# Optimization experiments

Hardware: AMD Instinct MI355X
Metric: run time of the kernel (lower is better)

The kernel has to match this reference:

```python
import jax, jax.numpy as jnp
from jax import lax
import numpy as np

ALPHA = 0.5   # combined weight on dice loss
BETA = 0.5    # combined weight on boundary loss; NOTE: BoundaryLoss also multiplies by beta internally, so boundary term gets beta**2 overall (faithful to the torch code)
SMOOTH = 1e-06
BIG = 1e6     # 'infinity' for 1D distance scans (>> H+W)


def _dist1d_last(mask):
    """1D distance (in pixels) to nearest True along the last axis of [B,H,W]."""
    m = jnp.moveaxis(mask, 2, 0)  # [W,B,H]
    init = jnp.full(m.shape[1:], jnp.float32(BIG))
    def step(c, mm):
        d = jnp.where(mm, jnp.float32(0.0), c + 1.0)
        return d, d
    _, fwd = lax.scan(step, init, m)
    _, bwd = lax.scan(step, init, m[::-1])
    g = jnp.minimum(fwd, bwd[::-1])
    return jnp.moveaxis(g, 0, 2)  # [B,H,W]


def _edt(mask):
    """Exact 2D Euclidean distance to nearest True pixel (Felzenszwalb-style separable pass).
    mask: [B,H,W] bool. Returns float32 [B,H,W].
    Phase 1: exact 1D distance along rows (two scans).
    Phase 2: per output row i, D2[i] = min_{i'} (i-i')^2 + g[i']^2 along columns.
    """
    g2 = _dist1d_last(mask) ** 2  # [B,H,W] squared row distances
    H = mask.shape[1]
    idx = jnp.arange(H, dtype=jnp.float32)
    def row(i):
        # min over source rows i' of g2[:, i', :] + (i - i')^2  -> [B,W]
        return jnp.min(g2 + ((i - idx) ** 2)[None, :, None], axis=1)
    d2 = lax.map(row, idx)  # [H,B,W]
    return jnp.sqrt(jnp.transpose(d2, (1, 0, 2)))  # [B,H,W]


def setup_inputs() -> dict:
    key = jax.random.key(0)
    k1, k2 = jax.random.split(key)
    inputs = jax.random.normal(k1, (16, 1, 512, 512), dtype=jnp.float32)
    targets = jax.random.randint(k2, (16, 1, 512, 512), 0, 2, dtype=jnp.int32)
    return {"inputs": inputs, "targets": targets}


def reference(inputs, targets):
    tf = targets.astype(jnp.float32)          # [B,1,H,W]
    t2d = tf[:, 0]                            # [B,H,W]
    probs_full = jax.nn.sigmoid(inputs)       # [B,1,H,W]
    probs = probs_full[:, 0]                  # [B,H,W]

    # BoundaryLoss: dist = EDT(t==0 input -> distance to nearest t==1) + EDT(t==1 input -> distance to nearest t==0)
    dist = _edt(t2d > 0.5) + _edt(t2d <= 0.5)
    loss_b = BETA * jnp.mean(probs * dist)    # internal beta of BoundaryLoss

    # DiceLoss (from_logits=True)
    intersection = jnp.sum(probs_full * tf)
    dice = (2.0 * intersection + SMOOTH) / (jnp.sum(probs_full) + jnp.sum(tf) + SMOOTH)
    loss_d = 1.0 - dice

    return ALPHA * loss_d + BETA * loss_b
```

## Files before the change

### kernel.cpp

```cpp
#include <hip/hip_runtime.h>
#include <math.h>

constexpr int B = 16, H = 512, W = 512;
constexpr int NPIX = B * H * W;
constexpr int ROWS = 8;
constexpr int HALO = 3;
constexpr int LROWS = ROWS + 2 * HALO;
constexpr int TPB = 512;
constexpr int NBLK = B * (H / ROWS);

#define ALPHA_C 0.5
#define BETA_C 0.5
#define SMOOTH_C 1e-06
#define BIGV 1000000.0f

__device__ inline double wave_reduce(double v) {
    #pragma unroll
    for (int off = 32; off > 0; off >>= 1)
        v += __shfl_down(v, off, 64);
    return v;
}

__device__ int row_nearest(const int* __restrict__ rowp, int c, bool oppOne) {
    for (int d = 0; d < W; ++d) {
        int l = c - d, r = c + d;
        if (l >= 0 && ((rowp[l] > 0) == oppOne)) return d;
        if (r <  W && ((rowp[r] > 0) == oppOne)) return d;
    }
    return 65535;
}

__global__ void __launch_bounds__(TPB, 4)
edt_fused_kernel(const float* __restrict__ logits,
                 const int* __restrict__ tgt,
                 double* __restrict__ partials) {
    __shared__ __align__(16) unsigned int gf[LROWS][W];
    __shared__ double sh[8][4];

    const int lane = threadIdx.x & 63;
    const int wv   = threadIdx.x >> 6;
    const int b    = blockIdx.x >> 6;
    const int r0   = (blockIdx.x & 63) * ROWS;
    const int* timg = tgt + (size_t)b * H * W;

    const float NEG = -(BIGV + 1.0f);
    const float POS = (float)W + BIGV;
    const float wbase = (float)(lane * 8);

    for (int s = wv; s < LROWS; s += 8) {
        const int grow = r0 - HALO + s;
        if (grow < 0 || grow >= H) {
            const uint4 sent = make_uint4(~0u, ~0u, ~0u, ~0u);
            *reinterpret_cast<uint4*>(&gf[s][lane * 8])     = sent;
            *reinterpret_cast<uint4*>(&gf[s][lane * 8 + 4]) = sent;
            continue;
        }
        const int* rowp = timg + (size_t)grow * W;
        const int4 t0 = *reinterpret_cast<const int4*>(rowp + lane * 8);
        const int4 t1 = *reinterpret_cast<const int4*>(rowp + lane * 8 + 4);
        bool m[8] = { t0.x > 0, t0.y > 0, t0.z > 0, t0.w > 0,
                      t1.x > 0, t1.y > 0, t1.z > 0, t1.w > 0 };

        float la = NEG, lb = NEG, ra = POS, rb = POS;
        #pragma unroll
        for (int j = 0; j < 8; ++j) {
            float w = wbase + (float)j;
            if (m[j]) la = w; else lb = w;
        }
        #pragma unroll
        for (int j = 7; j >= 0; --j) {
            float w = wbase + (float)j;
            if (m[j]) ra = w; else rb = w;
        }

        float sa = la, sb = lb;
        #pragma unroll
        for (int off = 1; off < 64; off <<= 1) {
            float ua = __shfl_up(sa, off, 64);
            float ub = __shfl_up(sb, off, 64);
            if (lane >= off) { sa = fmaxf(sa, ua); sb = fmaxf(sb, ub); }
        }
        float carry_a = __shfl_up(sa, 1, 64); if (lane == 0) carry_a = NEG;
        float carry_b = __shfl_up(sb, 1, 64); if (lane == 0) carry_b = NEG;

        float ta = ra, tb = rb;
        #pragma unroll
        for (int off = 1; off < 64; off <<= 1) {
            float ua = __shfl_down(ta, off, 64);
            float ub = __shfl_down(tb, off, 64);
            if (lane < 64 - off) { ta = fminf(ta, ua); tb = fminf(tb, ub); }
        }
        float rcarry_a = __shfl_down(ta, 1, 64); if (lane == 63) rcarry_a = POS;
        float rcarry_b = __shfl_down(tb, 1, 64); if (lane == 63) rcarry_b = POS;

        float ga[8], gb[8];
        la = carry_a; lb = carry_b;
        #pragma unroll
        for (int j = 0; j < 8; ++j) {
            float w = wbase + (float)j;
            if (m[j]) la = w; else lb = w;
            ga[j] = w - la;
            gb[j] = w - lb;
        }
        ra = rcarry_a; rb = rcarry_b;
        #pragma unroll
        for (int j = 7; j >= 0; --j) {
            float w = wbase + (float)j;
            if (m[j]) ra = w; else rb = w;
            ga[j] = fminf(ga[j], ra - w);
            gb[j] = fminf(gb[j], rb - w);
        }

        unsigned int pk[8];
        #pragma unroll
        for (int j = 0; j < 8; ++j) {
            unsigned int ua = (unsigned int)fminf(ga[j], 65535.0f);
            unsigned int ub = (unsigned int)fminf(gb[j], 65535.0f);
            pk[j] = ua | (ub << 16);
        }
        *reinterpret_cast<uint4*>(&gf[s][lane * 8])     = make_uint4(pk[0], pk[1], pk[2], pk[3]);
        *reinterpret_cast<uint4*>(&gf[s][lane * 8 + 4]) = make_uint4(pk[4], pk[5], pk[6], pk[7]);
    }
    __syncthreads();

    const int i  = r0 + wv;
    const int ci = wv + HALO;
    const int c0 = lane * 4;
    const size_t rowoff = (size_t)b * H * W + (size_t)i * W;

    const float4 lgA = *reinterpret_cast<const float4*>(logits + rowoff + c0);
    const float4 lgB = *reinterpret_cast<const float4*>(logits + rowoff + c0 + 256);
    const uint4  vA  = *reinterpret_cast<const uint4*>(&gf[ci][c0]);
    const uint4  vB  = *reinterpret_cast<const uint4*>(&gf[ci][c0 + 256]);

    const unsigned int va[8] = { vA.x, vA.y, vA.z, vA.w, vB.x, vB.y, vB.z, vB.w };
    const float xv[8] = { lgA.x, lgA.y, lgA.z, lgA.w, lgB.x, lgB.y, lgB.z, lgB.w };

    float best[8], tf[8];
    int shf[8];
    #pragma unroll
    for (int k = 0; k < 8; ++k) {
        bool t = ((va[k] & 0xffffu) == 0u);
        shf[k] = t ? 16 : 0;
        tf[k] = t ? 1.0f : 0.0f;
        float g = (float)((va[k] >> shf[k]) & 0xffffu);
        best[k] = g * g;
    }

    #pragma unroll
    for (int r = 1; r <= 3; ++r) {
        const float rr = (float)(r * r);
        const uint4 uA = *reinterpret_cast<const uint4*>(&gf[ci - r][c0]);
        const uint4 uB = *reinterpret_cast<const uint4*>(&gf[ci - r][c0 + 256]);
        const uint4 dA = *reinterpret_cast<const uint4*>(&gf[ci + r][c0]);
        const uint4 dB = *reinterpret_cast<const uint4*>(&gf[ci + r][c0 + 256]);
        const unsigned int au[8] = { uA.x, uA.y, uA.z, uA.w, uB.x, uB.y, uB.z, uB.w };
        const unsigned int ad[8] = { dA.x, dA.y, dA.z, dA.w, dB.x, dB.y, dB.z, dB.w };
        #pragma unroll
        for (int k = 0; k < 8; ++k) {
            float gu = (float)((au[k] >> shf[k]) & 0xffffu);
            float gd = (float)((ad[k] >> shf[k]) & 0xffffu);
            best[k] = fminf(best[k], fmaf(gu, gu, rr));
            best[k] = fminf(best[k], fmaf(gd, gd, rr));
        }
    }

    #pragma unroll
    for (int k = 0; k < 8; ++k) {
        if (best[k] > (float)(HALO + 1) * (HALO + 1)) {
            const int col = (k < 4) ? (c0 + k) : (c0 + 256 + k - 4);
            const bool oppOne = (tf[k] == 0.0f);
            for (int r = HALO + 1; r < H; ++r) {
                const float rr = (float)(r * r);
                if (rr >= best[k]) break;
                const int ju = i - r, jd = i + r;
                if (ju >= 0) {
                    float g = (float)row_nearest(timg + (size_t)ju * W, col, oppOne);
                    best[k] = fminf(best[k], fmaf(g, g, rr));
                }
                if (jd < H) {
                    float g = (float)row_nearest(timg + (size_t)jd * W, col, oppOne);
                    best[k] = fminf(best[k], fmaf(g, g, rr));
                }
            }
        }
    }

    double v_pd = 0.0, v_p = 0.0, v_t = 0.0, v_pt = 0.0;
    #pragma unroll
    for (int k = 0; k < 8; ++k) {
        const float dist = sqrtf(best[k]);
        const float p = 1.0f / (1.0f + __expf(-xv[k]));
        v_pd += (double)(p * dist);
        v_p  += (double)p;
        v_t  += (double)tf[k];
        v_pt += (double)(p * tf[k]);
    }

    v_pd = wave_reduce(v_pd);
    v_p  = wave_reduce(v_p);
    v_t  = wave_reduce(v_t);
    v_pt = wave_reduce(v_pt);

    if (lane == 0) {
        sh[wv][0] = v_pd; sh[wv][1] = v_p; sh[wv][2] = v_t; sh[wv][3] = v_pt;
    }
    __syncthreads();
    if (threadIdx.x == 0) {
        double s0 = 0.0, s1 = 0.0, s2 = 0.0, s3 = 0.0;
        #pragma unroll
        for (int q = 0; q < 8; ++q) {
            s0 += sh[q][0]; s1 += sh[q][1]; s2 += sh[q][2]; s3 += sh[q][3];
        }
        double* outp = partials + (size_t)blockIdx.x * 4;
        outp[0] = s0; outp[1] = s1; outp[2] = s2; outp[3] = s3;
    }
}

__global__ void finalize_kernel(const double* __restrict__ partials,
                                float* __restrict__ out) {
    double a0 = 0.0, a1 = 0.0, a2 = 0.0, a3 = 0.0;
    for (int j = threadIdx.x; j < NBLK; j += 256) {
        const double* p = partials + (size_t)j * 4;
        a0 += p[0]; a1 += p[1]; a2 += p[2]; a3 += p[3];
    }
    a0 = wave_reduce(a0);
    a1 = wave_reduce(a1);
    a2 = wave_reduce(a2);
    a3 = wave_reduce(a3);

    __shared__ double sh[4][4];
    const int wid = threadIdx.x >> 6, lane = threadIdx.x & 63;
    if (lane == 0) {
        sh[wid][0] = a0; sh[wid][1] = a1; sh[wid][2] = a2; sh[wid][3] = a3;
    }
    __syncthreads();
    if (threadIdx.x == 0) {
        double sum_pd = sh[0][0] + sh[1][0] + sh[2][0] + sh[3][0];
        double sum_p  = sh[0][1] + sh[1][1] + sh[2][1] + sh[3][1];
        double sum_t  = sh[0][2] + sh[1][2] + sh[2][2] + sh[3][2];
        double sum_pt = sh[0][3] + sh[1][3] + sh[2][3] + sh[3][3];

        double mean_pd = sum_pd / (double)NPIX;
        double loss_b = BETA_C * mean_pd;
        double dice = (2.0 * sum_pt + SMOOTH_C) / (sum_p + sum_t + SMOOTH_C);
        double loss_d = 1.0 - dice;
        out[0] = (float)(ALPHA_C * loss_d + BETA_C * loss_b);
    }
}

extern "C" void kernel_launch(void* const* d_in, const int* in_sizes, int n_in,
                              void* d_out, int out_size, void* d_ws, size_t ws_size,
                              hipStream_t stream) {
    const float* logits = (const float*)d_in[0];
    const int* tgt      = (const int*)d_in[1];
    float* out = (float*)d_out;

    double* partials = (double*)d_ws;

    edt_fused_kernel<<<NBLK, TPB, 0, stream>>>(logits, tgt, partials);
    finalize_kernel<<<1, 256, 0, stream>>>(partials, out);
}
```

Baseline: 24.92 us.

## Process 16 rows per block, use integer halo min and float reductions

Each block now covers 16 output rows instead of 8, so every wave handles two rows. This cuts the relative halo overhead (14 staged rows for 16 outputs instead of 8 outputs) and halves the block count. The 3-row halo minimum now runs in integer arithmetic, and the per-thread and per-wave accumulation uses float instead of double, keeping double only for the per-block partials. The risks are lower occupancy or parallelism from fewer blocks, and slightly reduced precision in the per-wave sums.

Result: faster. 22.35 us (-10.3%).

```diff
diff --git a/kernel.cpp b/kernel.cpp
--- a/kernel.cpp
+++ b/kernel.cpp
@@ -3,7 +3,7 @@
 
 constexpr int B = 16, H = 512, W = 512;
 constexpr int NPIX = B * H * W;
-constexpr int ROWS = 8;
+constexpr int ROWS = 16;
 constexpr int HALO = 3;
 constexpr int LROWS = ROWS + 2 * HALO;
 constexpr int TPB = 512;
@@ -14,7 +14,14 @@
 #define SMOOTH_C 1e-06
 #define BIGV 1000000.0f
 
-__device__ inline double wave_reduce(double v) {
+__device__ inline float wave_reduce_f(float v) {
+    #pragma unroll
+    for (int off = 32; off > 0; off >>= 1)
+        v += __shfl_down(v, off, 64);
+    return v;
+}
+
+__device__ inline double wave_reduce_d(double v) {
     #pragma unroll
     for (int off = 32; off > 0; off >>= 1)
         v += __shfl_down(v, off, 64);
@@ -39,8 +46,8 @@
 
     const int lane = threadIdx.x & 63;
     const int wv   = threadIdx.x >> 6;
-    const int b    = blockIdx.x >> 6;
-    const int r0   = (blockIdx.x & 63) * ROWS;
+    const int b    = blockIdx.x >> 5;
+    const int r0   = (blockIdx.x & 31) * ROWS;
     const int* timg = tgt + (size_t)b * H * W;
 
     const float NEG = -(BIGV + 1.0f);
@@ -123,87 +130,88 @@
     }
     __syncthreads();
 
-    const int i  = r0 + wv;
-    const int ci = wv + HALO;
+    float acc_pd = 0.0f, acc_p = 0.0f, acc_t = 0.0f, acc_pt = 0.0f;
     const int c0 = lane * 4;
-    const size_t rowoff = (size_t)b * H * W + (size_t)i * W;
-
-    const float4 lgA = *reinterpret_cast<const float4*>(logits + rowoff + c0);
-    const float4 lgB = *reinterpret_cast<const float4*>(logits + rowoff + c0 + 256);
-    const uint4  vA  = *reinterpret_cast<const uint4*>(&gf[ci][c0]);
-    const uint4  vB  = *reinterpret_cast<const uint4*>(&gf[ci][c0 + 256]);
-
-    const unsigned int va[8] = { vA.x, vA.y, vA.z, vA.w, vB.x, vB.y, vB.z, vB.w };
-    const float xv[8] = { lgA.x, lgA.y, lgA.z, lgA.w, lgB.x, lgB.y, lgB.z, lgB.w };
-
-    float best[8], tf[8];
-    int shf[8];
+
     #pragma unroll
-    for (int k = 0; k < 8; ++k) {
-        bool t = ((va[k] & 0xffffu) == 0u);
-        shf[k] = t ? 16 : 0;
-        tf[k] = t ? 1.0f : 0.0f;
-        float g = (float)((va[k] >> shf[k]) & 0xffffu);
-        best[k] = g * g;
-    }
-
-    #pragma unroll
-    for (int r = 1; r <= 3; ++r) {
-        const float rr = (float)(r * r);
-        const uint4 uA = *reinterpret_cast<const uint4*>(&gf[ci - r][c0]);
-        const uint4 uB = *reinterpret_cast<const uint4*>(&gf[ci - r][c0 + 256]);
-        const uint4 dA = *reinterpret_cast<const uint4*>(&gf[ci + r][c0]);
-        const uint4 dB = *reinterpret_cast<const uint4*>(&gf[ci + r][c0 + 256]);
-        const unsigned int au[8] = { uA.x, uA.y, uA.z, uA.w, uB.x, uB.y, uB.z, uB.w };
-        const unsigned int ad[8] = { dA.x, dA.y, dA.z, dA.w, dB.x, dB.y, dB.z, dB.w };
+    for (int half = 0; half < 2; ++half) {
+        const int i  = r0 + wv + half * 8;
+        const int ci = wv + half * 8 + HALO;
+        const size_t rowoff = (size_t)b * H * W + (size_t)i * W;
+
+        const float4 lgA = *reinterpret_cast<const float4*>(logits + rowoff + c0);
+        const float4 lgB = *reinterpret_cast<const float4*>(logits + rowoff + c0 + 256);
+        const uint4  vA  = *reinterpret_cast<const uint4*>(&gf[ci][c0]);
+        const uint4  vB  = *reinterpret_cast<const uint4*>(&gf[ci][c0 + 256]);
+
+        const unsigned int va[8] = { vA.x, vA.y, vA.z, vA.w, vB.x, vB.y, vB.z, vB.w };
+        const float xv[8] = { lgA.x, lgA.y, lgA.z, lgA.w, lgB.x, lgB.y, lgB.z, lgB.w };
+
+        unsigned int best[8], shf[8];
         #pragma unroll
         for (int k = 0; k < 8; ++k) {
-            float gu = (float)((au[k] >> shf[k]) & 0xffffu);
-            float gd = (float)((ad[k] >> shf[k]) & 0xffffu);
-            best[k] = fminf(best[k], fmaf(gu, gu, rr));
-            best[k] = fminf(best[k], fmaf(gd, gd, rr));
-        }
-    }
-
-    #pragma unroll
-    for (int k = 0; k < 8; ++k) {
-        if (best[k] > (float)(HALO + 1) * (HALO + 1)) {
-            const int col = (k < 4) ? (c0 + k) : (c0 + 256 + k - 4);
-            const bool oppOne = (tf[k] == 0.0f);
-            for (int r = HALO + 1; r < H; ++r) {
-                const float rr = (float)(r * r);
-                if (rr >= best[k]) break;
-                const int ju = i - r, jd = i + r;
-                if (ju >= 0) {
-                    float g = (float)row_nearest(timg + (size_t)ju * W, col, oppOne);
-                    best[k] = fminf(best[k], fmaf(g, g, rr));
-                }
-                if (jd < H) {
-                    float g = (float)row_nearest(timg + (size_t)jd * W, col, oppOne);
-                    best[k] = fminf(best[k], fmaf(g, g, rr));
+            bool t = ((va[k] & 0xffffu) == 0u);
+            shf[k] = t ? 16u : 0u;
+            unsigned int g = (va[k] >> shf[k]) & 0xffffu;
+            best[k] = g * g;
+        }
+
+        #pragma unroll
+        for (int r = 1; r <= 3; ++r) {
+            const unsigned int rr = (unsigned int)(r * r);
+            const uint4 uA = *reinterpret_cast<const uint4*>(&gf[ci - r][c0]);
+            const uint4 uB = *reinterpret_cast<const uint4*>(&gf[ci - r][c0 + 256]);
+            const uint4 dA = *reinterpret_cast<const uint4*>(&gf[ci + r][c0]);
+            const uint4 dB = *reinterpret_cast<const uint4*>(&gf[ci + r][c0 + 256]);
+            const unsigned int au[8] = { uA.x, uA.y, uA.z, uA.w, uB.x, uB.y, uB.z, uB.w };
+            const unsigned int ad[8] = { dA.x, dA.y, dA.z, dA.w, dB.x, dB.y, dB.z, dB.w };
+            #pragma unroll
+            for (int k = 0; k < 8; ++k) {
+                unsigned int gu = (au[k] >> shf[k]) & 0xffffu;
+                unsigned int gd = (ad[k] >> shf[k]) & 0xffffu;
+                best[k] = min(best[k], gu * gu + rr);
+                best[k] = min(best[k], gd * gd + rr);
+            }
+        }
+
+        #pragma unroll
+        for (int k = 0; k < 8; ++k) {
+            float bf = (float)best[k];
+            if (bf > 16.0f) {
+                const int col = (k < 4) ? (c0 + k) : (c0 + 256 + k - 4);
+                const bool oppOne = (shf[k] == 0u);
+                for (int r = HALO + 1; r < H; ++r) {
+                    const float rr = (float)(r * r);
+                    if (rr >= bf) break;
+                    const int ju = i - r, jd = i + r;
+                    if (ju >= 0) {
+                        float g = (float)row_nearest(timg + (size_t)ju * W, col, oppOne);
+                        bf = fminf(bf, fmaf(g, g, rr));
+                    }
+                    if (jd < H) {
+                        float g = (float)row_nearest(timg + (size_t)jd * W, col, oppOne);
+                        bf = fminf(bf, fmaf(g, g, rr));
+                    }
                 }
             }
-        }
-    }
-
-    double v_pd = 0.0, v_p = 0.0, v_t = 0.0, v_pt = 0.0;
-    #pragma unroll
-    for (int k = 0; k < 8; ++k) {
-        const float dist = sqrtf(best[k]);
-        const float p = 1.0f / (1.0f + __expf(-xv[k]));
-        v_pd += (double)(p * dist);
-        v_p  += (double)p;
-        v_t  += (double)tf[k];
-        v_pt += (double)(p * tf[k]);
-    }
-
-    v_pd = wave_reduce(v_pd);
-    v_p  = wave_reduce(v_p);
-    v_t  = wave_reduce(v_t);
-    v_pt = wave_reduce(v_pt);
+            const float dist = sqrtf(bf);
+            const float p = 1.0f / (1.0f + __expf(-xv[k]));
+            const float tfv = shf[k] ? 1.0f : 0.0f;
+            acc_pd += p * dist;
+            acc_p  += p;
+            acc_t  += tfv;
+            acc_pt = fmaf(tfv, p, acc_pt);
+        }
+    }
+
+    const float w_pd = wave_reduce_f(acc_pd);
+    const float w_p  = wave_reduce_f(acc_p);
+    const float w_t  = wave_reduce_f(acc_t);
+    const float w_pt = wave_reduce_f(acc_pt);
 
     if (lane == 0) {
-        sh[wv][0] = v_pd; sh[wv][1] = v_p; sh[wv][2] = v_t; sh[wv][3] = v_pt;
+        sh[wv][0] = (double)w_pd; sh[wv][1] = (double)w_p;
+        sh[wv][2] = (double)w_t;  sh[wv][3] = (double)w_pt;
     }
     __syncthreads();
     if (threadIdx.x == 0) {
@@ -224,10 +232,10 @@
         const double* p = partials + (size_t)j * 4;
         a0 += p[0]; a1 += p[1]; a2 += p[2]; a3 += p[3];
     }
-    a0 = wave_reduce(a0);
-    a1 = wave_reduce(a1);
-    a2 = wave_reduce(a2);
-    a3 = wave_reduce(a3);
+    a0 = wave_reduce_d(a0);
+    a1 = wave_reduce_d(a1);
+    a2 = wave_reduce_d(a2);
+    a3 = wave_reduce_d(a3);
 
     __shared__ double sh[4][4];
     const int wid = threadIdx.x >> 6, lane = threadIdx.x & 63;
```
